# Optimization experiments

Hardware: AMD Instinct MI355X
Metric: run time of the kernel (lower is better)

Reference implementation:

```python
import jax, jax.numpy as jnp
import numpy as np

EPS = 1e-20

def efficient_squash(s):
    # Efficient-CapsNet squash: (1 - 1/e^||s||) * s/||s||
    n = jnp.linalg.norm(s, axis=-1, keepdims=True)
    return (1.0 - 1.0 / (jnp.exp(n) + EPS)) * (s / (n + EPS))

def setup_inputs() -> dict:
    key = jax.random.key(0)
    k1, k2 = jax.random.split(key)
    B, N, D_in = 32, 2048, 16
    K, D_out = 32, 16
    x = jax.random.normal(k1, (B, N, D_in), dtype=jnp.float32)
    # he_normal fan_in = N * D_in * ... ; use simple scaled normal init
    w = jax.random.normal(k2, (K, N, D_in, D_out), dtype=jnp.float32) * 0.05
    b = jnp.zeros((K, N, 1), dtype=jnp.float32)
    return {"x": x, "w": w, "b": b}

def reference(x, w, b):
    D_out = w.shape[-1]
    # projection: [B,N,D_in] x [K,N,D_in,D_out] -> [B,K,N,D_out]
    u = jnp.einsum('bji,kjiz->bkjz', x, w)
    # agreement c_{bkj} = sum_{i,z} u_{bkjz} u_{bkiz} = <u_j, sum_i u_i>
    t = jnp.sum(u, axis=2)                      # [B,K,D_out]
    c = jnp.einsum('bkjz,bkz->bkj', u, t)[..., None]  # [B,K,N,1]
    c = c / jnp.sqrt(jnp.asarray(D_out, jnp.float32))
    c = jax.nn.softmax(c, axis=1)               # softmax over capsules K
    c = c + b                                   # broadcast [K,N,1]
    s = jnp.sum(u * c, axis=2)                  # [B,K,D_out]
    return efficient_squash(s)
```

## Files before the change

kernel.cpp:

```cpp
#include <hip/hip_runtime.h>

#define NN 2048
#define KK 32

typedef __attribute__((ext_vector_type(8))) short short8;
typedef __attribute__((ext_vector_type(4))) float f32x4;

#define WS_U     0UL
#define WS_TPART 67108864UL
#define WS_TP2   100663296UL
#define WS_T     101711872UL
#define WS_SPART 101777408UL
#define WS_NEED  105971712UL

__device__ __forceinline__ float bf_lo(unsigned v) { return __uint_as_float(v << 16); }
__device__ __forceinline__ float bf_hi(unsigned v) { return __uint_as_float(v & 0xffff0000u); }
__device__ __forceinline__ unsigned pack_bf16(float a, float b) {
    unsigned ua = __float_as_uint(a), ub = __float_as_uint(b);
    return ((ua + 0x8000u) >> 16) | ((ub + 0x8000u) & 0xffff0000u);
}
__device__ __forceinline__ short8 pack8(const float* r) {
    short8 o;
#pragma unroll
    for (int e = 0; e < 8; ++e)
        o[e] = (short)(unsigned short)((__float_as_uint(r[e]) + 0x8000u) >> 16);
    return o;
}
__device__ __forceinline__ short8 sel8(bool keep, short8 v) {
    union { short8 s; unsigned u[4]; } a, b;
    a.s = v;
#pragma unroll
    for (int i = 0; i < 4; ++i) b.u[i] = keep ? a.u[i] : 0u;
    return b.s;
}

__global__ __launch_bounds__(512)
void kA2(const float* __restrict__ x, const float* __restrict__ w,
         unsigned* __restrict__ u_pk, float* __restrict__ t_part)
{
    const int tid = threadIdx.x;
    const int wv = tid >> 6, l = tid & 63;
    const int c16 = l & 15, g = l >> 4;
    const int jl = g >> 1, ih = g & 1;
    const int j0 = blockIdx.x * 4;

    f32x4 T[4][2];
#pragma unroll
    for (int ckl = 0; ckl < 4; ++ckl)
#pragma unroll
        for (int bn = 0; bn < 2; ++bn) T[ckl][bn] = (f32x4){0.f, 0.f, 0.f, 0.f};

#pragma unroll
    for (int p = 0; p < 2; ++p) {
        const int jp = j0 + p * 2 + jl;

        short8 Wf[4];
#pragma unroll
        for (int ckl = 0; ckl < 4; ++ckl) {
            const int k = wv * 4 + ckl;
            const float* wp = w + ((size_t)k * NN + jp) * 256 + ih * 128 + c16;
            float br[8];
#pragma unroll
            for (int e = 0; e < 8; ++e) br[e] = wp[e * 16];
            Wf[ckl] = pack8(br);
        }
        short8 Xf[2];
#pragma unroll
        for (int bn = 0; bn < 2; ++bn) {
            const float* xp = x + ((size_t)(bn * 16 + c16) * NN + jp) * 16 + ih * 8;
            float ar[8];
            float4 v0 = *reinterpret_cast<const float4*>(xp);
            float4 v1 = *reinterpret_cast<const float4*>(xp + 4);
            ar[0]=v0.x; ar[1]=v0.y; ar[2]=v0.z; ar[3]=v0.w;
            ar[4]=v1.x; ar[5]=v1.y; ar[6]=v1.z; ar[7]=v1.w;
            Xf[bn] = pack8(ar);
        }

#pragma unroll
        for (int jj = 0; jj < 2; ++jj) {
            const bool keep = (jl == jj);
            const int j = j0 + p * 2 + jj;
            const f32x4 zero = (f32x4){0.f, 0.f, 0.f, 0.f};
#pragma unroll
            for (int ckl = 0; ckl < 4; ++ckl) {
                const int k = wv * 4 + ckl;
                const short8 wsel = sel8(keep, Wf[ckl]);
#pragma unroll
                for (int bn = 0; bn < 2; ++bn) {
                    f32x4 Cj = __builtin_amdgcn_mfma_f32_16x16x32_bf16(
                        wsel, Xf[bn], zero, 0, 0, 0);
                    T[ckl][bn] += Cj;
                    uint2 o;
                    o.x = pack_bf16(Cj[0], Cj[1]);
                    o.y = pack_bf16(Cj[2], Cj[3]);
                    *reinterpret_cast<uint2*>(u_pk +
                        (((size_t)j * 32 + bn * 16 + c16) * 32 + k) * 8 + g * 2) = o;
                }
            }
        }
    }

    float* tp = t_part + (size_t)blockIdx.x * 16384;
#pragma unroll
    for (int ckl = 0; ckl < 4; ++ckl)
#pragma unroll
        for (int bn = 0; bn < 2; ++bn)
            *reinterpret_cast<f32x4*>(tp + (bn * 16 + c16) * 512 +
                                      (wv * 4 + ckl) * 16 + g * 4) = T[ckl][bn];
}

__global__ __launch_bounds__(256)
void kred32(const float* __restrict__ src, float* __restrict__ dst)
{
    const int idx = blockIdx.x * 256 + threadIdx.x;
    const int c4 = idx & 4095, ch = idx >> 12;
    const f32x4* P = reinterpret_cast<const f32x4*>(src);
    f32x4 a0 = (f32x4){0,0,0,0}, a1 = a0, a2 = a0, a3 = a0;
#pragma unroll 2
    for (int q = 0; q < 32; q += 4) {
        a0 += P[(size_t)(ch * 32 + q + 0) * 4096 + c4];
        a1 += P[(size_t)(ch * 32 + q + 1) * 4096 + c4];
        a2 += P[(size_t)(ch * 32 + q + 2) * 4096 + c4];
        a3 += P[(size_t)(ch * 32 + q + 3) * 4096 + c4];
    }
    reinterpret_cast<f32x4*>(dst)[(size_t)ch * 4096 + c4] = (a0 + a1) + (a2 + a3);
}

__global__ __launch_bounds__(256)
void kt2(const float* __restrict__ tp2, float* __restrict__ t)
{
    const int c4 = blockIdx.x * 256 + threadIdx.x;
    const f32x4* P = reinterpret_cast<const f32x4*>(tp2);
    f32x4 a0 = (f32x4){0,0,0,0}, a1 = a0, a2 = a0, a3 = a0;
#pragma unroll
    for (int q = 0; q < 16; q += 4) {
        a0 += P[(size_t)(q + 0) * 4096 + c4];
        a1 += P[(size_t)(q + 1) * 4096 + c4];
        a2 += P[(size_t)(q + 2) * 4096 + c4];
        a3 += P[(size_t)(q + 3) * 4096 + c4];
    }
    reinterpret_cast<f32x4*>(t)[c4] = (a0 + a1) + (a2 + a3);
}

__global__ __launch_bounds__(256)
void kB2(const unsigned* __restrict__ u_pk, const float* __restrict__ t,
         const float* __restrict__ bias, float* __restrict__ s_part)
{
    __shared__ float lc_lds[32][33];
    __shared__ float s_lds[8][32][16];
    const int tid = threadIdx.x;
    const int k   = tid & 31;
    const int jl  = tid >> 5;
    const int b   = blockIdx.x >> 6;
    const int jc  = blockIdx.x & 63;

    float tr[16];
    const float4* tp = reinterpret_cast<const float4*>(t + ((size_t)b * KK + k) * 16);
#pragma unroll
    for (int q = 0; q < 4; ++q) {
        float4 v = tp[q];
        tr[4 * q + 0] = v.x; tr[4 * q + 1] = v.y; tr[4 * q + 2] = v.z; tr[4 * q + 3] = v.w;
    }

    uint4 ua[4], ud[4];
#pragma unroll
    for (int jj = 0; jj < 4; ++jj) {
        const int jL = jj * 8 + jl;
        const int jg = jc * 32 + jL;
        const uint4* up = reinterpret_cast<const uint4*>(u_pk)
                        + (((size_t)jg * 32 + b) * 32 + k) * 2;
        ua[jj] = up[0]; ud[jj] = up[1];
        float a0 = 0.f, a1 = 0.f;
        a0 = fmaf(bf_lo(ua[jj].x), tr[0],  a0); a1 = fmaf(bf_hi(ua[jj].x), tr[1],  a1);
        a0 = fmaf(bf_lo(ua[jj].y), tr[2],  a0); a1 = fmaf(bf_hi(ua[jj].y), tr[3],  a1);
        a0 = fmaf(bf_lo(ua[jj].z), tr[4],  a0); a1 = fmaf(bf_hi(ua[jj].z), tr[5],  a1);
        a0 = fmaf(bf_lo(ua[jj].w), tr[6],  a0); a1 = fmaf(bf_hi(ua[jj].w), tr[7],  a1);
        a0 = fmaf(bf_lo(ud[jj].x), tr[8],  a0); a1 = fmaf(bf_hi(ud[jj].x), tr[9],  a1);
        a0 = fmaf(bf_lo(ud[jj].y), tr[10], a0); a1 = fmaf(bf_hi(ud[jj].y), tr[11], a1);
        a0 = fmaf(bf_lo(ud[jj].z), tr[12], a0); a1 = fmaf(bf_hi(ud[jj].z), tr[13], a1);
        a0 = fmaf(bf_lo(ud[jj].w), tr[14], a0); a1 = fmaf(bf_hi(ud[jj].w), tr[15], a1);
        lc_lds[jL][k] = a0 + a1;
    }
    __syncthreads();

    {
        const int jq = tid >> 3, kq = tid & 7;
        float lv[4];
#pragma unroll
        for (int m = 0; m < 4; ++m) lv[m] = lc_lds[jq][kq * 4 + m];
        float pm = fmaxf(fmaxf(lv[0], lv[1]), fmaxf(lv[2], lv[3]));
        pm = fmaxf(pm, __shfl_xor(pm, 1));
        pm = fmaxf(pm, __shfl_xor(pm, 2));
        pm = fmaxf(pm, __shfl_xor(pm, 4));
        float ev[4], ps = 0.f;
#pragma unroll
        for (int m = 0; m < 4; ++m) { ev[m] = __expf((lv[m] - pm) * 0.25f); ps += ev[m]; }
        ps += __shfl_xor(ps, 1);
        ps += __shfl_xor(ps, 2);
        ps += __shfl_xor(ps, 4);
        const float inv = 1.f / ps;
        const int jg = jc * 32 + jq;
#pragma unroll
        for (int m = 0; m < 4; ++m)
            lv[m] = ev[m] * inv + bias[(size_t)(kq * 4 + m) * NN + jg];
        __syncthreads();
#pragma unroll
        for (int m = 0; m < 4; ++m) lc_lds[jq][kq * 4 + m] = lv[m];
    }
    __syncthreads();

    float sacc[16];
#pragma unroll
    for (int z = 0; z < 16; ++z) sacc[z] = 0.f;
#pragma unroll
    for (int jj = 0; jj < 4; ++jj) {
        const float cv = lc_lds[jj * 8 + jl][k];
        const uint4 a = ua[jj], d = ud[jj];
        sacc[0]  = fmaf(cv, bf_lo(a.x), sacc[0]);  sacc[1]  = fmaf(cv, bf_hi(a.x), sacc[1]);
        sacc[2]  = fmaf(cv, bf_lo(a.y), sacc[2]);  sacc[3]  = fmaf(cv, bf_hi(a.y), sacc[3]);
        sacc[4]  = fmaf(cv, bf_lo(a.z), sacc[4]);  sacc[5]  = fmaf(cv, bf_hi(a.z), sacc[5]);
        sacc[6]  = fmaf(cv, bf_lo(a.w), sacc[6]);  sacc[7]  = fmaf(cv, bf_hi(a.w), sacc[7]);
        sacc[8]  = fmaf(cv, bf_lo(d.x), sacc[8]);  sacc[9]  = fmaf(cv, bf_hi(d.x), sacc[9]);
        sacc[10] = fmaf(cv, bf_lo(d.y), sacc[10]); sacc[11] = fmaf(cv, bf_hi(d.y), sacc[11]);
        sacc[12] = fmaf(cv, bf_lo(d.z), sacc[12]); sacc[13] = fmaf(cv, bf_hi(d.z), sacc[13]);
        sacc[14] = fmaf(cv, bf_lo(d.w), sacc[14]); sacc[15] = fmaf(cv, bf_hi(d.w), sacc[15]);
    }

#pragma unroll
    for (int q = 0; q < 4; ++q)
        *reinterpret_cast<float4*>(&s_lds[jl][k][q * 4]) =
            make_float4(sacc[q * 4], sacc[q * 4 + 1], sacc[q * 4 + 2], sacc[q * 4 + 3]);
    __syncthreads();
    {
        const int kk = tid >> 3, zp = tid & 7;
        float2 o; o.x = 0.f; o.y = 0.f;
#pragma unroll
        for (int l2 = 0; l2 < 8; ++l2) {
            o.x += s_lds[l2][kk][2 * zp];
            o.y += s_lds[l2][kk][2 * zp + 1];
        }
        reinterpret_cast<float2*>(s_part)[((size_t)b * 64 + jc) * 256 + kk * 8 + zp] = o;
    }
}

__global__ __launch_bounds__(256)
void k4_squash(const float* __restrict__ s_part, float* __restrict__ out)
{
    const int idx4 = blockIdx.x * 256 + threadIdx.x;
    const int b = idx4 >> 7, loc4 = idx4 & 127;
    const float4* p = reinterpret_cast<const float4*>(s_part) + (size_t)b * 8192 + loc4;
    float4 s = make_float4(0.f, 0.f, 0.f, 0.f);
#pragma unroll 8
    for (int jc = 0; jc < 64; ++jc) {
        float4 v = p[jc * 128];
        s.x += v.x; s.y += v.y; s.z += v.z; s.w += v.w;
    }
    float ss = s.x * s.x + s.y * s.y + s.z * s.z + s.w * s.w;
    ss += __shfl_xor(ss, 1);
    ss += __shfl_xor(ss, 2);
    const float n = sqrtf(ss);
    const float sc = (1.f - 1.f / (__expf(n) + 1e-20f)) / (n + 1e-20f);
    float4 o; o.x = s.x * sc; o.y = s.y * sc; o.z = s.z * sc; o.w = s.w * sc;
    reinterpret_cast<float4*>(out)[idx4] = o;
}

__global__ void k_sentinel(float* __restrict__ out)
{
    out[blockIdx.x * 256 + threadIdx.x] = 12345.0f;
}

extern "C" void kernel_launch(void* const* d_in, const int* in_sizes, int n_in,
                              void* d_out, int out_size, void* d_ws, size_t ws_size,
                              hipStream_t stream)
{
    const float* x    = (const float*)d_in[0];
    const float* w    = (const float*)d_in[1];
    const float* bias = (const float*)d_in[2];
    float* out        = (float*)d_out;

    char* ws = (char*)d_ws;
    if (ws_size < WS_NEED) {
        k_sentinel<<<dim3(64), dim3(256), 0, stream>>>(out);
        return;
    }
    unsigned* u_pk = (unsigned*)(ws + WS_U);
    float* t_part  = (float*)(ws + WS_TPART);
    float* tp2     = (float*)(ws + WS_TP2);
    float* t       = (float*)(ws + WS_T);
    float* s_part  = (float*)(ws + WS_SPART);

    kA2      <<<dim3(512),  dim3(512), 0, stream>>>(x, w, u_pk, t_part);
    kred32   <<<dim3(256),  dim3(256), 0, stream>>>(t_part, tp2);
    kt2      <<<dim3(16),   dim3(256), 0, stream>>>(tp2, t);
    kB2      <<<dim3(2048), dim3(256), 0, stream>>>(u_pk, t, bias, s_part);
    k4_squash<<<dim3(16),   dim3(256), 0, stream>>>(s_part, out);
}
```

Before: 67.31 us.

## Stage u stores through LDS and compute t by re-reading bf16 u

The projection kernel no longer keeps per-block fp32 partial sums of t. It now handles two j per block instead of four, doubling the grid, and routes its bf16 u outputs through a padded LDS buffer so the global stores are coalesced. A new reduction kernel sums the packed bf16 u tensor over N in two stages to produce t, replacing the 32 MB partial-sum write and its two reduction passes. The trade-off is a full extra read of the 64 MB u buffer, and t is now summed from bf16-rounded values rather than fp32 accumulators.

```diff
diff --git a/kernel.cpp b/kernel.cpp
--- a/kernel.cpp
+++ b/kernel.cpp
@@ -7,11 +7,10 @@
 typedef __attribute__((ext_vector_type(4))) float f32x4;
 
 #define WS_U     0UL
-#define WS_TPART 67108864UL
-#define WS_TP2   100663296UL
-#define WS_T     101711872UL
-#define WS_SPART 101777408UL
-#define WS_NEED  105971712UL
+#define WS_TP3   67108864UL
+#define WS_T     67633152UL
+#define WS_SPART 67698688UL
+#define WS_NEED  71892992UL
 
 __device__ __forceinline__ float bf_lo(unsigned v) { return __uint_as_float(v << 16); }
 __device__ __forceinline__ float bf_hi(unsigned v) { return __uint_as_float(v & 0xffff0000u); }
@@ -36,110 +35,111 @@
 
 __global__ __launch_bounds__(512)
 void kA2(const float* __restrict__ x, const float* __restrict__ w,
-         unsigned* __restrict__ u_pk, float* __restrict__ t_part)
-{
+         unsigned* __restrict__ u_pk)
+{
+    __shared__ uint2 xfer[8][2][32][17];
     const int tid = threadIdx.x;
     const int wv = tid >> 6, l = tid & 63;
     const int c16 = l & 15, g = l >> 4;
     const int jl = g >> 1, ih = g & 1;
-    const int j0 = blockIdx.x * 4;
-
-    f32x4 T[4][2];
-#pragma unroll
-    for (int ckl = 0; ckl < 4; ++ckl)
-#pragma unroll
-        for (int bn = 0; bn < 2; ++bn) T[ckl][bn] = (f32x4){0.f, 0.f, 0.f, 0.f};
-
-#pragma unroll
-    for (int p = 0; p < 2; ++p) {
-        const int jp = j0 + p * 2 + jl;
-
-        short8 Wf[4];
+    const int j0 = blockIdx.x * 2;
+    const int jp = j0 + jl;
+
+    short8 Wf[4];
+#pragma unroll
+    for (int ckl = 0; ckl < 4; ++ckl) {
+        const int k = wv * 4 + ckl;
+        const float* wp = w + ((size_t)k * NN + jp) * 256 + ih * 128 + c16;
+        float br[8];
+#pragma unroll
+        for (int e = 0; e < 8; ++e) br[e] = wp[e * 16];
+        Wf[ckl] = pack8(br);
+    }
+    short8 Xf[2];
+#pragma unroll
+    for (int bn = 0; bn < 2; ++bn) {
+        const float* xp = x + ((size_t)(bn * 16 + c16) * NN + jp) * 16 + ih * 8;
+        float ar[8];
+        float4 v0 = *reinterpret_cast<const float4*>(xp);
+        float4 v1 = *reinterpret_cast<const float4*>(xp + 4);
+        ar[0]=v0.x; ar[1]=v0.y; ar[2]=v0.z; ar[3]=v0.w;
+        ar[4]=v1.x; ar[5]=v1.y; ar[6]=v1.z; ar[7]=v1.w;
+        Xf[bn] = pack8(ar);
+    }
+
+#pragma unroll
+    for (int jj = 0; jj < 2; ++jj) {
+        const bool keep = (jl == jj);
+        const f32x4 zero = (f32x4){0.f, 0.f, 0.f, 0.f};
+        uint2* xw = &xfer[wv][jj][0][0];
 #pragma unroll
         for (int ckl = 0; ckl < 4; ++ckl) {
-            const int k = wv * 4 + ckl;
-            const float* wp = w + ((size_t)k * NN + jp) * 256 + ih * 128 + c16;
-            float br[8];
-#pragma unroll
-            for (int e = 0; e < 8; ++e) br[e] = wp[e * 16];
-            Wf[ckl] = pack8(br);
-        }
-        short8 Xf[2];
-#pragma unroll
-        for (int bn = 0; bn < 2; ++bn) {
-            const float* xp = x + ((size_t)(bn * 16 + c16) * NN + jp) * 16 + ih * 8;
-            float ar[8];
-            float4 v0 = *reinterpret_cast<const float4*>(xp);
-            float4 v1 = *reinterpret_cast<const float4*>(xp + 4);
-            ar[0]=v0.x; ar[1]=v0.y; ar[2]=v0.z; ar[3]=v0.w;
-            ar[4]=v1.x; ar[5]=v1.y; ar[6]=v1.z; ar[7]=v1.w;
-            Xf[bn] = pack8(ar);
-        }
-
-#pragma unroll
-        for (int jj = 0; jj < 2; ++jj) {
-            const bool keep = (jl == jj);
-            const int j = j0 + p * 2 + jj;
-            const f32x4 zero = (f32x4){0.f, 0.f, 0.f, 0.f};
-#pragma unroll
-            for (int ckl = 0; ckl < 4; ++ckl) {
-                const int k = wv * 4 + ckl;
-                const short8 wsel = sel8(keep, Wf[ckl]);
-#pragma unroll
-                for (int bn = 0; bn < 2; ++bn) {
-                    f32x4 Cj = __builtin_amdgcn_mfma_f32_16x16x32_bf16(
-                        wsel, Xf[bn], zero, 0, 0, 0);
-                    T[ckl][bn] += Cj;
-                    uint2 o;
-                    o.x = pack_bf16(Cj[0], Cj[1]);
-                    o.y = pack_bf16(Cj[2], Cj[3]);
-                    *reinterpret_cast<uint2*>(u_pk +
-                        (((size_t)j * 32 + bn * 16 + c16) * 32 + k) * 8 + g * 2) = o;
-                }
+            const short8 wsel = sel8(keep, Wf[ckl]);
+#pragma unroll
+            for (int bn = 0; bn < 2; ++bn) {
+                f32x4 Cj = __builtin_amdgcn_mfma_f32_16x16x32_bf16(
+                    wsel, Xf[bn], zero, 0, 0, 0);
+                uint2 o;
+                o.x = pack_bf16(Cj[0], Cj[1]);
+                o.y = pack_bf16(Cj[2], Cj[3]);
+                xw[(bn * 16 + c16) * 17 + ckl * 4 + g] = o;
             }
         }
     }
 
-    float* tp = t_part + (size_t)blockIdx.x * 16384;
-#pragma unroll
-    for (int ckl = 0; ckl < 4; ++ckl)
-#pragma unroll
-        for (int bn = 0; bn < 2; ++bn)
-            *reinterpret_cast<f32x4*>(tp + (bn * 16 + c16) * 512 +
-                                      (wv * 4 + ckl) * 16 + g * 4) = T[ckl][bn];
+#pragma unroll
+    for (int jj = 0; jj < 2; ++jj) {
+        const uint2* xw = &xfer[wv][jj][0][0];
+        uint2* ubase = reinterpret_cast<uint2*>(u_pk)
+                     + (size_t)(j0 + jj) * 4096 + wv * 16 + c16;
+#pragma unroll
+        for (int m = 0; m < 8; ++m) {
+            uint2 v = xw[(m * 4 + g) * 17 + c16];
+            ubase[m * 512 + g * 128] = v;
+        }
+    }
+}
+
+__global__ __launch_bounds__(1024)
+void kt_u(const unsigned* __restrict__ u_pk, float2* __restrict__ t_part3)
+{
+    __shared__ float2 red[4][256];
+    const int tid = threadIdx.x;
+    const int js4 = tid >> 8, cl = tid & 255;
+    const int cc  = blockIdx.x & 31, jsl = blockIdx.x >> 5;
+    const int col = cc * 256 + cl;
+
+    const unsigned* up = u_pk + (size_t)(jsl * 256 + js4) * 8192 + col;
+    float a_lo = 0.f, a_hi = 0.f;
+#pragma unroll 4
+    for (int q = 0; q < 64; ++q) {
+        unsigned v = up[(size_t)q * 4 * 8192];
+        a_lo += bf_lo(v); a_hi += bf_hi(v);
+    }
+    red[js4][cl] = make_float2(a_lo, a_hi);
+    __syncthreads();
+    if (tid < 256) {
+        float2 r0 = red[0][tid], r1 = red[1][tid], r2 = red[2][tid], r3 = red[3][tid];
+        float2 o;
+        o.x = (r0.x + r1.x) + (r2.x + r3.x);
+        o.y = (r0.y + r1.y) + (r2.y + r3.y);
+        t_part3[(size_t)jsl * 8192 + cc * 256 + tid] = o;
+    }
 }
 
 __global__ __launch_bounds__(256)
-void kred32(const float* __restrict__ src, float* __restrict__ dst)
-{
-    const int idx = blockIdx.x * 256 + threadIdx.x;
-    const int c4 = idx & 4095, ch = idx >> 12;
-    const f32x4* P = reinterpret_cast<const f32x4*>(src);
-    f32x4 a0 = (f32x4){0,0,0,0}, a1 = a0, a2 = a0, a3 = a0;
-#pragma unroll 2
-    for (int q = 0; q < 32; q += 4) {
-        a0 += P[(size_t)(ch * 32 + q + 0) * 4096 + c4];
-        a1 += P[(size_t)(ch * 32 + q + 1) * 4096 + c4];
-        a2 += P[(size_t)(ch * 32 + q + 2) * 4096 + c4];
-        a3 += P[(size_t)(ch * 32 + q + 3) * 4096 + c4];
-    }
-    reinterpret_cast<f32x4*>(dst)[(size_t)ch * 4096 + c4] = (a0 + a1) + (a2 + a3);
-}
-
-__global__ __launch_bounds__(256)
-void kt2(const float* __restrict__ tp2, float* __restrict__ t)
-{
-    const int c4 = blockIdx.x * 256 + threadIdx.x;
-    const f32x4* P = reinterpret_cast<const f32x4*>(tp2);
-    f32x4 a0 = (f32x4){0,0,0,0}, a1 = a0, a2 = a0, a3 = a0;
-#pragma unroll
-    for (int q = 0; q < 16; q += 4) {
-        a0 += P[(size_t)(q + 0) * 4096 + c4];
-        a1 += P[(size_t)(q + 1) * 4096 + c4];
-        a2 += P[(size_t)(q + 2) * 4096 + c4];
-        a3 += P[(size_t)(q + 3) * 4096 + c4];
-    }
-    reinterpret_cast<f32x4*>(t)[c4] = (a0 + a1) + (a2 + a3);
+void kt2b(const float2* __restrict__ t_part3, float* __restrict__ t)
+{
+    const int cidx = blockIdx.x * 256 + threadIdx.x;
+    float2 a = make_float2(0.f, 0.f);
+#pragma unroll
+    for (int sl = 0; sl < 8; ++sl) {
+        float2 v = t_part3[(size_t)sl * 8192 + cidx];
+        a.x += v.x; a.y += v.y;
+    }
+    const int b = cidx >> 8, k = (cidx >> 3) & 31, zp = cidx & 7;
+    t[(size_t)(b * 32 + k) * 16 + zp * 2]     = a.x;
+    t[(size_t)(b * 32 + k) * 16 + zp * 2 + 1] = a.y;
 }
 
 __global__ __launch_bounds__(256)
@@ -283,15 +283,14 @@
         k_sentinel<<<dim3(64), dim3(256), 0, stream>>>(out);
         return;
     }
-    unsigned* u_pk = (unsigned*)(ws + WS_U);
-    float* t_part  = (float*)(ws + WS_TPART);
-    float* tp2     = (float*)(ws + WS_TP2);
-    float* t       = (float*)(ws + WS_T);
-    float* s_part  = (float*)(ws + WS_SPART);
-
-    kA2      <<<dim3(512),  dim3(512), 0, stream>>>(x, w, u_pk, t_part);
-    kred32   <<<dim3(256),  dim3(256), 0, stream>>>(t_part, tp2);
-    kt2      <<<dim3(16),   dim3(256), 0, stream>>>(tp2, t);
-    kB2      <<<dim3(2048), dim3(256), 0, stream>>>(u_pk, t, bias, s_part);
-    k4_squash<<<dim3(16),   dim3(256), 0, stream>>>(s_part, out);
-}
+    unsigned* u_pk   = (unsigned*)(ws + WS_U);
+    float2*   t_part3= (float2*)(ws + WS_TP3);
+    float*    t      = (float*)(ws + WS_T);
+    float*    s_part = (float*)(ws + WS_SPART);
+
+    kA2      <<<dim3(1024), dim3(512),  0, stream>>>(x, w, u_pk);
+    kt_u     <<<dim3(256),  dim3(1024), 0, stream>>>(u_pk, t_part3);
+    kt2b     <<<dim3(32),   dim3(256),  0, stream>>>(t_part3, t);
+    kB2      <<<dim3(2048), dim3(256),  0, stream>>>(u_pk, t, bias, s_part);
+    k4_squash<<<dim3(16),   dim3(256),  0, stream>>>(s_part, out);
+}
```

After: 63.32 us. -5.9%, faster.
